# Performance work log

Measured on AMD Instinct MI355X. Metric: run time of the kernel, lower is better.

The kernel has to match this reference:

```python
import jax, jax.numpy as jnp
import numpy as np

B, LAT, H, OUT, S, L = 256, 128, 256, 64, 512, 2


def _lstm_layer(xs, h0, c0, Wih, Whh, bih, bhh):
    # xs: [B, S, in_dim]; PyTorch gate order i, f, g, o
    gx = jnp.einsum('bsi,gi->bsg', xs, Wih) + bih + bhh  # [B,S,4H], precomputed input proj
    gx = jnp.swapaxes(gx, 0, 1)  # [S,B,4H]

    def step(carry, g_t):
        h, c = carry
        g = g_t + h @ Whh.T
        i, f, gg, o = jnp.split(g, 4, axis=-1)
        i, f, o = jax.nn.sigmoid(i), jax.nn.sigmoid(f), jax.nn.sigmoid(o)
        c = f * c + i * jnp.tanh(gg)
        h = o * jnp.tanh(c)
        return (h, c), h

    (_, _), hs = jax.lax.scan(step, (h0, c0), gx)
    return jnp.swapaxes(hs, 0, 1)  # [B,S,H]


def setup_inputs() -> dict:
    key = jax.random.key(0)
    ks = jax.random.split(key, 20)
    sc = 0.05
    d = {
        'z': jax.random.normal(ks[0], (B, LAT), jnp.float32),
        'fc_hidden_w': jax.random.normal(ks[1], (H * L, LAT), jnp.float32) * sc,
        'fc_hidden_b': jnp.zeros((H * L,), jnp.float32),
        'fc_cell_w': jax.random.normal(ks[2], (H * L, LAT), jnp.float32) * sc,
        'fc_cell_b': jnp.zeros((H * L,), jnp.float32),
        'fc_input_w': jax.random.normal(ks[3], (H, LAT), jnp.float32) * sc,
        'fc_input_b': jnp.zeros((H,), jnp.float32),
        'W_ih0': jax.random.normal(ks[4], (4 * H, H), jnp.float32) * sc,
        'W_hh0': jax.random.normal(ks[5], (4 * H, H), jnp.float32) * sc,
        'b_ih0': jnp.zeros((4 * H,), jnp.float32),
        'b_hh0': jnp.zeros((4 * H,), jnp.float32),
        'W_ih1': jax.random.normal(ks[6], (4 * H, H), jnp.float32) * sc,
        'W_hh1': jax.random.normal(ks[7], (4 * H, H), jnp.float32) * sc,
        'b_ih1': jnp.zeros((4 * H,), jnp.float32),
        'b_hh1': jnp.zeros((4 * H,), jnp.float32),
        'fc_output_w': jax.random.normal(ks[8], (OUT, H), jnp.float32) * sc,
        'fc_output_b': jnp.zeros((OUT,), jnp.float32),
    }
    return d


def reference(z, fc_hidden_w, fc_hidden_b, fc_cell_w, fc_cell_b, fc_input_w, fc_input_b,
              W_ih0, W_hh0, b_ih0, b_hh0, W_ih1, W_hh1, b_ih1, b_hh1,
              fc_output_w, fc_output_b):
    # init hidden/cell per layer: view(B, L, H) -> layer axis first
    hidden = (z @ fc_hidden_w.T + fc_hidden_b).reshape(B, L, H)
    cell = (z @ fc_cell_w.T + fc_cell_b).reshape(B, L, H)
    # repeated decoder input (same vector at every timestep)
    x0 = z @ fc_input_w.T + fc_input_b  # [B,H]
    xs = jnp.broadcast_to(x0[:, None, :], (B, S, H))
    h1 = _lstm_layer(xs, hidden[:, 0], cell[:, 0], W_ih0, W_hh0, b_ih0, b_hh0)
    # dropout between layers is inference no-op
    h2 = _lstm_layer(h1, hidden[:, 1], cell[:, 1], W_ih1, W_hh1, b_ih1, b_hh1)
    return h2 @ fc_output_w.T + fc_output_b  # [B,S,OUT]
```

## Files before the change

### kernel.cpp

```cpp
#include <hip/hip_runtime.h>
#include <hip/hip_bf16.h>

#define LAT 128
#define H 256
#define OUTD 64
#define SEQ 512

typedef short bf16x8 __attribute__((ext_vector_type(8)));
typedef float f32x4  __attribute__((ext_vector_type(4)));
typedef unsigned long long u64;
typedef unsigned u32;

__device__ __forceinline__ float sigm(float x)  { return 1.f / (1.f + __expf(-x)); }
__device__ __forceinline__ float tanhf_(float x){ return 1.f - 2.f / (__expf(2.f * x) + 1.f); }

__device__ __forceinline__ short f2bs(float x) {
    __hip_bfloat16 b = __float2bfloat16(x);
    return *reinterpret_cast<short*>(&b);
}
__device__ __forceinline__ float bs2f(unsigned short h) {
    u32 b = ((u32)h) << 16;
    float f; __builtin_memcpy(&f, &b, 4); return f;
}
__device__ __forceinline__ u32 f2pair(float a, float b) {
    return ((u32)(unsigned short)f2bs(b) << 16) | (u32)(unsigned short)f2bs(a);
}
__device__ __forceinline__ bf16x8 pack8(const float* s) {
    bf16x8 v;
    v[0]=f2bs(s[0]); v[1]=f2bs(s[1]); v[2]=f2bs(s[2]); v[3]=f2bs(s[3]);
    v[4]=f2bs(s[4]); v[5]=f2bs(s[5]); v[6]=f2bs(s[6]); v[7]=f2bs(s[7]);
    return v;
}

__device__ __forceinline__ u64 sys_load_u64(const u64* p) {
    return __hip_atomic_load((u64*)p, __ATOMIC_RELAXED, __HIP_MEMORY_SCOPE_SYSTEM);
}
__device__ __forceinline__ void sys_store_u64(u64* p, u64 v) {
    __hip_atomic_store(p, v, __ATOMIC_RELAXED, __HIP_MEMORY_SCOPE_SYSTEM);
}

__global__ void lstm_prologue_init(const float* __restrict__ z,
                                   const float* __restrict__ Whid,
                                   const float* __restrict__ bhid,
                                   const float* __restrict__ Wcell,
                                   const float* __restrict__ bcell,
                                   const float* __restrict__ bih1,
                                   const float* __restrict__ bhh1,
                                   u64* __restrict__ h0B1,
                                   u64* __restrict__ h1B1,
                                   float* __restrict__ c0,
                                   float* __restrict__ c1,
                                   float* __restrict__ gxb1)
{
    int t = blockIdx.x * 256 + threadIdx.x;
    if (t < 65536) {
        int layer = t >> 15;
        int tt = t & 32767;
        int b = tt >> 7, cp = tt & 127;
        int colA = layer * H + 2 * cp;
        const float* zr = z + b * LAT;
        const float* wA = Whid + colA * LAT;
        const float* wB = wA + LAT;
        float a0 = bhid[colA], a1 = bhid[colA + 1];
        for (int k = 0; k < LAT; k++) { float zv = zr[k]; a0 += zv * wA[k]; a1 += zv * wB[k]; }
        u64 v = ((u64)(u32)layer << 32) | (u64)f2pair(a0, a1);
        (layer ? h1B1 : h0B1)[b * 128 + cp] = v;
    } else if (t < 196608) {
        int tt = t - 65536;
        int b = tt >> 9, col = tt & 511;
        const float* w  = Wcell + col * LAT;
        const float* zr = z + b * LAT;
        float acc = bcell[col];
        for (int k = 0; k < LAT; k++) acc += zr[k] * w[k];
        if (col < H) c0[b * H + col] = acc;
        else         c1[b * H + (col - H)] = acc;
    } else if (t < 197632) {
        int g = t - 196608;
        gxb1[g] = bih1[g] + bhh1[g];
    }
}

__global__ void lstm_prologue_gx0(const float* __restrict__ z,
                                  const float* __restrict__ Win,
                                  const float* __restrict__ bin,
                                  const float* __restrict__ Wih0,
                                  const float* __restrict__ bih0,
                                  const float* __restrict__ bhh0,
                                  u32* __restrict__ gxb0u)
{
    __shared__ float xs[H];
    const int b = blockIdx.y;
    const int tid = threadIdx.x;
    {
        const float* w  = Win + tid * LAT;
        const float* zr = z + b * LAT;
        float acc = bin[tid];
        for (int k = 0; k < LAT; k++) acc += zr[k] * w[k];
        xs[tid] = acc;
    }
    __syncthreads();
    const int cA = blockIdx.x * 512 + 2 * tid;
    const float* wA = Wih0 + cA * H;
    const float* wB = wA + H;
    float a0 = bih0[cA]     + bhh0[cA];
    float a1 = bih0[cA + 1] + bhh0[cA + 1];
    for (int k = 0; k < H; k++) { float xv = xs[k]; a0 += xv * wA[k]; a1 += xv * wB[k]; }
    gxb0u[b * 512 + blockIdx.x * 256 + tid] = f2pair(a0, a1);
}

__global__ __launch_bounds__(256, 1)
void lstm_persistent(const u32* __restrict__ gxb0u, const float* __restrict__ gxb1,
                     const float* __restrict__ c0g, const float* __restrict__ c1g,
                     u64* __restrict__ h0B0, u64* __restrict__ h0B1,
                     u64* __restrict__ h1B0, u64* __restrict__ h1B1,
                     const float* __restrict__ Whh0, const float* __restrict__ Wih1,
                     const float* __restrict__ Whh1, const float* __restrict__ Wout,
                     const float* __restrict__ bout, float* __restrict__ out)
{
    const int wg = blockIdx.x;
    const int bg = wg >> 4;
    const int j  = wg & 15;
    const int tid  = threadIdx.x;
    const int wave = tid >> 6;
    const int q  = (tid >> 4) & 3;
    const int ln = tid & 15;
    const int mycol = j * 16 + wave * 4 + q;
    const int myb   = bg * 16 + ln;

    __shared__ u32 hs0[2][16 * 132];
    __shared__ u32 hs1[2][16 * 132];

    bf16x8 wf[3][8];
    {
        const float* mats[3] = { Whh0, Wih1, Whh1 };
        const int arow = (ln & 3) * H + j * 16 + wave * 4 + (ln >> 2);
        #pragma unroll
        for (int mm = 0; mm < 3; mm++) {
            const float* s = mats[mm] + arow * H;
            #pragma unroll
            for (int kk = 0; kk < 8; kk++) wf[mm][kk] = pack8(s + kk * 32 + q * 8);
        }
    }
    const bool doOut = (j < 4) && (wave == 0);
    bf16x8 wo[8];
    float bor[4] = {0.f, 0.f, 0.f, 0.f};
    if (doOut) {
        const int orow = j * 16 + ln;
        const float* s = Wout + orow * H;
        #pragma unroll
        for (int kk = 0; kk < 8; kk++) wo[kk] = pack8(s + kk * 32 + q * 8);
        #pragma unroll
        for (int r = 0; r < 4; r++) bor[r] = bout[j * 16 + q * 4 + r];
    }

    float gxr0[4], gxr1[4];
    #pragma unroll
    for (int r = 0; r < 4; r++) {
        u32 v = gxb0u[myb * 512 + ((r * 256 + mycol) >> 1)];
        gxr0[r] = bs2f((unsigned short)((mycol & 1) ? (v >> 16) : (v & 0xFFFFu)));
        gxr1[r] = gxb1[r * 256 + mycol];
    }
    float creg0 = c0g[myb * H + mycol];
    float creg1 = c1g[myb * H + mycol];

    u64* A0 = h0B0 + bg * 2048;
    u64* A1 = h0B1 + bg * 2048;
    u64* B0 = h1B0 + bg * 2048;
    u64* B1 = h1B1 + bg * 2048;

    const int pubslot = ln * 128 + j * 8 + wave * 2 + (q >> 1);
    const bool pubLane = ((q & 1) == 0);

    for (int k = 0; k <= SEQ + 1; k++) {
        const u64* P0 = (k & 1) ? A0 : A1;  u64* C0 = (k & 1) ? A1 : A0;
        const u64* P1 = (k & 1) ? B1 : B0;  u64* C1 = (k & 1) ? B0 : B1;
        const int par = k & 1;

        if (k <= SEQ) {
            u64 v[8];
            bool ok = false; int guard = 0;
            while (!ok && guard < 16384) {
                ok = true;
                #pragma unroll
                for (int i = 0; i < 8; i++) v[i] = sys_load_u64(P0 + i * 256 + tid);
                #pragma unroll
                for (int i = 0; i < 8; i++) ok = ok && ((u32)(v[i] >> 32) == (u32)k);
                guard++;
            }
            u32* dst = hs0[par];
            #pragma unroll
            for (int i = 0; i < 8; i++) { int s = i * 256 + tid; dst[(s >> 7) * 132 + (s & 127)] = (u32)v[i]; }
        }
        __syncthreads();

        bf16x8 hb0[8];
        {
            const unsigned short* b0p = (const unsigned short*)hs0[par];
            #pragma unroll
            for (int kk = 0; kk < 8; kk++)
                hb0[kk] = *(const bf16x8*)(b0p + ln * 264 + kk * 32 + q * 8);
        }

        if (k < SEQ) {
            f32x4 acc = {0.f, 0.f, 0.f, 0.f};
            #pragma unroll
            for (int kk = 0; kk < 8; kk++)
                acc = __builtin_amdgcn_mfma_f32_16x16x32_bf16(wf[0][kk], hb0[kk], acc, 0, 0, 0);
            float i_ = sigm(acc[0] + gxr0[0]);
            float f_ = sigm(acc[1] + gxr0[1]);
            float g_ = tanhf_(acc[2] + gxr0[2]);
            float o_ = sigm(acc[3] + gxr0[3]);
            creg0 = f_ * creg0 + i_ * g_;
            int us = (int)(u32)(unsigned short)f2bs(o_ * tanhf_(creg0));
            int other = __shfl_xor(us, 16);
            if (pubLane) {
                u32 pa = (u32)us | ((u32)other << 16);
                sys_store_u64(C0 + pubslot, ((u64)(u32)(k + 1) << 32) | (u64)pa);
            }
        }

        if (k >= 1) {
            u64 v[8];
            bool ok = false; int guard = 0;
            while (!ok && guard < 16384) {
                ok = true;
                #pragma unroll
                for (int i = 0; i < 8; i++) v[i] = sys_load_u64(P1 + i * 256 + tid);
                #pragma unroll
                for (int i = 0; i < 8; i++) ok = ok && ((u32)(v[i] >> 32) == (u32)k);
                guard++;
            }
            u32* dst = hs1[par];
            #pragma unroll
            for (int i = 0; i < 8; i++) { int s = i * 256 + tid; dst[(s >> 7) * 132 + (s & 127)] = (u32)v[i]; }
        }
        __syncthreads();

        bf16x8 hb1[8];
        {
            const unsigned short* b1p = (const unsigned short*)hs1[par];
            #pragma unroll
            for (int kk = 0; kk < 8; kk++)
                hb1[kk] = *(const bf16x8*)(b1p + ln * 264 + kk * 32 + q * 8);
        }

        if (k >= 1 && k <= SEQ) {
            f32x4 acc = {0.f, 0.f, 0.f, 0.f};
            #pragma unroll
            for (int kk = 0; kk < 8; kk++)
                acc = __builtin_amdgcn_mfma_f32_16x16x32_bf16(wf[1][kk], hb0[kk], acc, 0, 0, 0);
            #pragma unroll
            for (int kk = 0; kk < 8; kk++)
                acc = __builtin_amdgcn_mfma_f32_16x16x32_bf16(wf[2][kk], hb1[kk], acc, 0, 0, 0);
            float i_ = sigm(acc[0] + gxr1[0]);
            float f_ = sigm(acc[1] + gxr1[1]);
            float g_ = tanhf_(acc[2] + gxr1[2]);
            float o_ = sigm(acc[3] + gxr1[3]);
            creg1 = f_ * creg1 + i_ * g_;
            int us = (int)(u32)(unsigned short)f2bs(o_ * tanhf_(creg1));
            int other = __shfl_xor(us, 16);
            if (pubLane) {
                u32 pa = (u32)us | ((u32)other << 16);
                sys_store_u64(C1 + pubslot, ((u64)(u32)(k + 1) << 32) | (u64)pa);
            }
        }

        if (k >= 2 && doOut) {
            f32x4 acc = {0.f, 0.f, 0.f, 0.f};
            #pragma unroll
            for (int kk = 0; kk < 8; kk++)
                acc = __builtin_amdgcn_mfma_f32_16x16x32_bf16(wo[kk], hb1[kk], acc, 0, 0, 0);
            f32x4 res;
            #pragma unroll
            for (int r = 0; r < 4; r++) res[r] = acc[r] + bor[r];
            *(f32x4*)&out[(bg * 16 + ln) * (SEQ * OUTD) + (k - 2) * OUTD + j * 16 + q * 4] = res;
        }
    }
}

extern "C" void kernel_launch(void* const* d_in, const int* in_sizes, int n_in,
                              void* d_out, int out_size, void* d_ws, size_t ws_size,
                              hipStream_t stream) {
    const float* z     = (const float*)d_in[0];
    const float* Whid  = (const float*)d_in[1];
    const float* bhid  = (const float*)d_in[2];
    const float* Wcell = (const float*)d_in[3];
    const float* bcell = (const float*)d_in[4];
    const float* Win   = (const float*)d_in[5];
    const float* bin   = (const float*)d_in[6];
    const float* Wih0  = (const float*)d_in[7];
    const float* Whh0  = (const float*)d_in[8];
    const float* bih0  = (const float*)d_in[9];
    const float* bhh0  = (const float*)d_in[10];
    const float* Wih1  = (const float*)d_in[11];
    const float* Whh1  = (const float*)d_in[12];
    const float* bih1  = (const float*)d_in[13];
    const float* bhh1  = (const float*)d_in[14];
    const float* Wout  = (const float*)d_in[15];
    const float* bout  = (const float*)d_in[16];
    float* out = (float*)d_out;

    u32*   gxb0u = (u32*)d_ws;
    float* gxb1  = (float*)(gxb0u + 131072);
    float* c0    = gxb1 + 1024;
    float* c1    = c0 + 65536;
    u64*   h0B0  = (u64*)(c1 + 65536);
    u64*   h0B1  = h0B0 + 32768;
    u64*   h1B0  = h0B1 + 32768;
    u64*   h1B1  = h1B0 + 32768;

    lstm_prologue_init<<<772, 256, 0, stream>>>(z, Whid, bhid, Wcell, bcell,
                                                bih1, bhh1, h0B1, h1B1, c0, c1, gxb1);
    lstm_prologue_gx0<<<dim3(2, 256), 256, 0, stream>>>(z, Win, bin, Wih0, bih0, bhh0, gxb0u);

    void* kargs[] = { (void*)&gxb0u, (void*)&gxb1, (void*)&c0, (void*)&c1,
                      (void*)&h0B0, (void*)&h0B1, (void*)&h1B0, (void*)&h1B1,
                      (void*)&Whh0, (void*)&Wih1, (void*)&Whh1, (void*)&Wout,
                      (void*)&bout, (void*)&out };
    hipError_t ce = hipLaunchCooperativeKernel((const void*)lstm_persistent,
                                               dim3(256), dim3(256), kargs, 0, stream);
    if (ce != hipSuccess) {
        lstm_persistent<<<256, 256, 0, stream>>>(gxb0u, gxb1, c0, c1,
                                                 h0B0, h0B1, h1B0, h1B1,
                                                 Whh0, Wih1, Whh1, Wout, bout, out);
    }
}
```

Measured before the change: 1.564 ms.

## Merge per-step barriers and prefetch next-step hidden-state polls early

The two polling phases (layer 0 and layer 1 hidden states) are merged under a single __syncthreads per timestep instead of two. The layer-1 load is issued before the layer-0 wait so both global reads are in flight together. The next step's layer-0 buffer is also speculatively loaded right after publishing, so the flag check often succeeds without another round trip. This cuts barrier count and polling latency on the serial recurrence critical path. The cost is extra registers and possibly stale speculative reads that must be re-polled.

```diff
diff --git a/kernel.cpp b/kernel.cpp
--- a/kernel.cpp
+++ b/kernel.cpp
@@ -171,25 +171,56 @@
     const int pubslot = ln * 128 + j * 8 + wave * 2 + (q >> 1);
     const bool pubLane = ((q & 1) == 0);
 
+    u64 v0[8];
+    #pragma unroll
+    for (int i = 0; i < 8; i++) v0[i] = sys_load_u64(A1 + i * 256 + tid);
+
     for (int k = 0; k <= SEQ + 1; k++) {
-        const u64* P0 = (k & 1) ? A0 : A1;  u64* C0 = (k & 1) ? A1 : A0;
         const u64* P1 = (k & 1) ? B1 : B0;  u64* C1 = (k & 1) ? B0 : B1;
+        u64* C0 = (k & 1) ? A1 : A0;
         const int par = k & 1;
 
+        u64 v1[8];
+        if (k >= 1) {
+            #pragma unroll
+            for (int i = 0; i < 8; i++) v1[i] = sys_load_u64(P1 + i * 256 + tid);
+        }
+
         if (k <= SEQ) {
-            u64 v[8];
-            bool ok = false; int guard = 0;
+            const u64* P0 = (k & 1) ? A0 : A1;
+            bool ok = true;
+            #pragma unroll
+            for (int i = 0; i < 8; i++) ok = ok && ((u32)(v0[i] >> 32) == (u32)k);
+            int guard = 0;
             while (!ok && guard < 16384) {
                 ok = true;
                 #pragma unroll
-                for (int i = 0; i < 8; i++) v[i] = sys_load_u64(P0 + i * 256 + tid);
+                for (int i = 0; i < 8; i++) v0[i] = sys_load_u64(P0 + i * 256 + tid);
                 #pragma unroll
-                for (int i = 0; i < 8; i++) ok = ok && ((u32)(v[i] >> 32) == (u32)k);
+                for (int i = 0; i < 8; i++) ok = ok && ((u32)(v0[i] >> 32) == (u32)k);
                 guard++;
             }
             u32* dst = hs0[par];
             #pragma unroll
-            for (int i = 0; i < 8; i++) { int s = i * 256 + tid; dst[(s >> 7) * 132 + (s & 127)] = (u32)v[i]; }
+            for (int i = 0; i < 8; i++) { int s = i * 256 + tid; dst[(s >> 7) * 132 + (s & 127)] = (u32)v0[i]; }
+        }
+
+        if (k >= 1) {
+            bool ok = true;
+            #pragma unroll
+            for (int i = 0; i < 8; i++) ok = ok && ((u32)(v1[i] >> 32) == (u32)k);
+            int guard = 0;
+            while (!ok && guard < 16384) {
+                ok = true;
+                #pragma unroll
+                for (int i = 0; i < 8; i++) v1[i] = sys_load_u64(P1 + i * 256 + tid);
+                #pragma unroll
+                for (int i = 0; i < 8; i++) ok = ok && ((u32)(v1[i] >> 32) == (u32)k);
+                guard++;
+            }
+            u32* dst = hs1[par];
+            #pragma unroll
+            for (int i = 0; i < 8; i++) { int s = i * 256 + tid; dst[(s >> 7) * 132 + (s & 127)] = (u32)v1[i]; }
         }
         __syncthreads();
 
@@ -199,6 +230,13 @@
             #pragma unroll
             for (int kk = 0; kk < 8; kk++)
                 hb0[kk] = *(const bf16x8*)(b0p + ln * 264 + kk * 32 + q * 8);
+        }
+        bf16x8 hb1[8];
+        {
+            const unsigned short* b1p = (const unsigned short*)hs1[par];
+            #pragma unroll
+            for (int kk = 0; kk < 8; kk++)
+                hb1[kk] = *(const bf16x8*)(b1p + ln * 264 + kk * 32 + q * 8);
         }
 
         if (k < SEQ) {
@@ -219,31 +257,6 @@
             }
         }
 
-        if (k >= 1) {
-            u64 v[8];
-            bool ok = false; int guard = 0;
-            while (!ok && guard < 16384) {
-                ok = true;
-                #pragma unroll
-                for (int i = 0; i < 8; i++) v[i] = sys_load_u64(P1 + i * 256 + tid);
-                #pragma unroll
-                for (int i = 0; i < 8; i++) ok = ok && ((u32)(v[i] >> 32) == (u32)k);
-                guard++;
-            }
-            u32* dst = hs1[par];
-            #pragma unroll
-            for (int i = 0; i < 8; i++) { int s = i * 256 + tid; dst[(s >> 7) * 132 + (s & 127)] = (u32)v[i]; }
-        }
-        __syncthreads();
-
-        bf16x8 hb1[8];
-        {
-            const unsigned short* b1p = (const unsigned short*)hs1[par];
-            #pragma unroll
-            for (int kk = 0; kk < 8; kk++)
-                hb1[kk] = *(const bf16x8*)(b1p + ln * 264 + kk * 32 + q * 8);
-        }
-
         if (k >= 1 && k <= SEQ) {
             f32x4 acc = {0.f, 0.f, 0.f, 0.f};
             #pragma unroll
@@ -263,6 +276,11 @@
                 u32 pa = (u32)us | ((u32)other << 16);
                 sys_store_u64(C1 + pubslot, ((u64)(u32)(k + 1) << 32) | (u64)pa);
             }
+        }
+
+        if (k < SEQ) {
+            #pragma unroll
+            for (int i = 0; i < 8; i++) v0[i] = sys_load_u64(C0 + i * 256 + tid);
         }
 
         if (k >= 2 && doOut) {
```

New measurement: 1.851 ms. +18.3%, slower.
